# Performance work log

Measured on AMD Instinct MI355X. Metric: run time of the kernel, lower is better.

Reference implementation:

```python
import jax, jax.numpy as jnp
import numpy as np

N, E, IN_DIM, H, C, ED = 100000, 1600000, 128, 8, 16, 16
LN_EPS = 1e-5


def setup_inputs() -> dict:
    key = jax.random.key(0)
    ks = jax.random.split(key, 12)
    s_in = 1.0 / np.sqrt(IN_DIM)
    s_ed = 1.0 / np.sqrt(ED)
    return {
        "edge_index": jax.random.randint(ks[0], (2, E), 0, N, dtype=jnp.int64),
        "point_attr": jax.random.normal(ks[1], (N, IN_DIM), dtype=jnp.float32),
        "edge_attr": jax.random.normal(ks[2], (E, ED), dtype=jnp.float32),
        "W": jax.random.normal(ks[3], (IN_DIM, H * C), dtype=jnp.float32) * s_in,
        "att_src": jax.random.normal(ks[4], (1, H, C), dtype=jnp.float32) * 0.1,
        "att_dst": jax.random.normal(ks[5], (1, H, C), dtype=jnp.float32) * 0.1,
        "W_edge": jax.random.normal(ks[6], (ED, H * C), dtype=jnp.float32) * s_ed,
        "att_edge": jax.random.normal(ks[7], (1, H, C), dtype=jnp.float32) * 0.1,
        "bias": jnp.zeros((H * C,), dtype=jnp.float32),
        "ln_node_g": jnp.ones((H * C,), dtype=jnp.float32),
        "ln_node_b": jnp.zeros((H * C,), dtype=jnp.float32),
        "ln_edge_g": jnp.ones((H,), dtype=jnp.float32),
        "ln_edge_b": jnp.zeros((H,), dtype=jnp.float32),
        "edge_w": jax.random.normal(ks[8], (H, 1), dtype=jnp.float32) / np.sqrt(H),
        "edge_b": jnp.zeros((1,), dtype=jnp.float32),
    }


def _layer_norm(x, g, b):
    mu = jnp.mean(x, axis=-1, keepdims=True)
    var = jnp.mean((x - mu) ** 2, axis=-1, keepdims=True)
    return (x - mu) * jax.lax.rsqrt(var + LN_EPS) * g + b


def reference(edge_index, point_attr, edge_attr, W, att_src, att_dst, W_edge,
              att_edge, bias, ln_node_g, ln_node_b, ln_edge_g, ln_edge_b,
              edge_w, edge_b):
    src, dst = edge_index[0], edge_index[1]
    x = (point_attr @ W).reshape(N, H, C)                 # [N,H,C]
    a_src = jnp.sum(x * att_src, axis=-1)                 # [N,H]
    a_dst = jnp.sum(x * att_dst, axis=-1)                 # [N,H]
    e = (edge_attr @ W_edge).reshape(E, H, C)             # [E,H,C]
    a_edge = jnp.sum(e * att_edge, axis=-1)               # [E,H]
    alpha = jax.nn.leaky_relu(a_src[src] + a_dst[dst] + a_edge, 0.2)
    # segment softmax over destination neighborhoods
    m = jax.ops.segment_max(alpha, dst, num_segments=N)
    m = jnp.where(jnp.isfinite(m), m, 0.0)
    ex = jnp.exp(alpha - m[dst])
    den = jax.ops.segment_sum(ex, dst, num_segments=N)
    alpha_n = ex / (den[dst] + 1e-16)                     # [E,H]
    msg = x[src] * alpha_n[..., None]                     # [E,H,C]
    out = jax.ops.segment_sum(msg, dst, num_segments=N).reshape(N, H * C) + bias
    node_out = jax.nn.leaky_relu(_layer_norm(out, ln_node_g, ln_node_b), 0.01)
    edge_h = _layer_norm(alpha_n, ln_edge_g, ln_edge_b)
    edge_out = jax.nn.relu(edge_h @ edge_w + edge_b)[:, 0]  # [E]
    return node_out, edge_out
```

## Files before the change

kernel.cpp:

```cpp
#include <hip/hip_runtime.h>
#include <hip/hip_bf16.h>

#define NN 100000
#define EE 1600000
#define LN_EPS 1e-5f

__device__ __forceinline__ float bf_lo(unsigned u) {
  union { unsigned i; float f; } c; c.i = u << 16; return c.f;
}
__device__ __forceinline__ float bf_hi(unsigned u) {
  union { unsigned i; float f; } c; c.i = u & 0xffff0000u; return c.f;
}
__device__ __forceinline__ float us_bf(unsigned short u) {
  union { unsigned i; float f; } c; c.i = ((unsigned)u) << 16; return c.f;
}
__device__ __forceinline__ unsigned short f2bf(float f) {
  union { float f; unsigned i; } c; c.f = f;
  unsigned b = c.i + 0x7fffu + ((c.i >> 16) & 1u);
  return (unsigned short)(b >> 16);
}
__device__ __forceinline__ float lrelu02(float v) { return v >= 0.f ? v : 0.2f * v; }

__global__ void k_detect(const void* __restrict__ ei, int* __restrict__ flag) {
  if (threadIdx.x == 0 && blockIdx.x == 0) {
    const unsigned long long* p = (const unsigned long long*)ei;
    int ok = 1;
    for (int i = 0; i < 256; ++i)
      if (p[i] >= (unsigned long long)NN) { ok = 0; break; }
    *flag = ok;
  }
}

__global__ __launch_bounds__(256) void k_convert_hist(const void* __restrict__ ei,
                                                      const int* __restrict__ flag,
                                                      int* __restrict__ idx32,
                                                      int* __restrict__ counts) {
  int gid = blockIdx.x * 256 + threadIdx.x;
  if (gid >= EE) return;
  int i0 = gid * 2;
  int v0, v1;
  if (*flag) {
    longlong2 lv = *(const longlong2*)((const long long*)ei + i0);
    v0 = (int)lv.x; v1 = (int)lv.y;
  } else {
    int2 iv = *(const int2*)((const int*)ei + i0);
    v0 = iv.x; v1 = iv.y;
  }
  *(int2*)(idx32 + i0) = make_int2(v0, v1);
  if (i0 >= EE) {
    atomicAdd(&counts[v0], 1);
    atomicAdd(&counts[v1], 1);
  }
}

__global__ __launch_bounds__(512) void k_gemm_node(
    const float* __restrict__ P, const float* __restrict__ W,
    const float* __restrict__ attS, const float* __restrict__ attD,
    unsigned* __restrict__ xb, unsigned short* __restrict__ a_srcb,
    unsigned short* __restrict__ a_dstb, int nrows) {
  __shared__ float Rl[32 * 66];
  int t = threadIdx.x;
  int w = __builtin_amdgcn_readfirstlane(t >> 6);
  int l = t & 63;
  int rb = blockIdx.x * 64;
  int cb = w * 16;
  float acc[16];
#pragma unroll
  for (int j = 0; j < 16; ++j) acc[j] = 0.f;

  for (int kc = 0; kc < 4; ++kc) {
    __syncthreads();
    {
      int row = t >> 3;
      int k0 = (t & 7) * 4;
      int grow = rb + row;
      float4 v = make_float4(0.f, 0.f, 0.f, 0.f);
      if (grow < nrows)
        v = *(const float4*)(P + (size_t)grow * 128 + kc * 32 + k0);
      Rl[(k0 + 0) * 66 + row] = v.x;
      Rl[(k0 + 1) * 66 + row] = v.y;
      Rl[(k0 + 2) * 66 + row] = v.z;
      Rl[(k0 + 3) * 66 + row] = v.w;
    }
    __syncthreads();
    const float* Wp = W + (size_t)(kc * 32) * 128 + cb;
#pragma unroll 8
    for (int k = 0; k < 32; ++k) {
      float rv = Rl[k * 66 + l];
#pragma unroll
      for (int j = 0; j < 16; ++j) acc[j] = fmaf(rv, Wp[k * 128 + j], acc[j]);
    }
  }
  int row = rb + l;
  if (row < nrows) {
    float sa = 0.f, sd = 0.f;
#pragma unroll
    for (int j = 0; j < 16; ++j) {
      sa = fmaf(acc[j], attS[cb + j], sa);
      sd = fmaf(acc[j], attD[cb + j], sd);
    }
    a_srcb[(size_t)row * 8 + w] = f2bf(sa);
    a_dstb[(size_t)row * 8 + w] = f2bf(sd);
    unsigned pk[8];
#pragma unroll
    for (int m = 0; m < 8; ++m)
      pk[m] = (unsigned)f2bf(acc[2 * m]) | ((unsigned)f2bf(acc[2 * m + 1]) << 16);
    unsigned* xo = xb + (size_t)row * 64 + cb / 2;
    *(uint4*)(xo) = make_uint4(pk[0], pk[1], pk[2], pk[3]);
    *(uint4*)(xo + 4) = make_uint4(pk[4], pk[5], pk[6], pk[7]);
  }
}

__global__ __launch_bounds__(256) void k_blocksum(const int* __restrict__ counts,
                                                  int* __restrict__ partials, int n) {
  __shared__ int sm[256];
  int t = threadIdx.x;
  int gid = blockIdx.x * 256 + t;
  sm[t] = gid < n ? counts[gid] : 0;
  __syncthreads();
  for (int s = 128; s > 0; s >>= 1) {
    if (t < s) sm[t] += sm[t + s];
    __syncthreads();
  }
  if (t == 0) partials[blockIdx.x] = sm[0];
}

__global__ __launch_bounds__(512) void k_scanpartials(int* __restrict__ partials, int nb) {
  __shared__ int sm[512];
  int t = threadIdx.x;
  int v = t < nb ? partials[t] : 0;
  sm[t] = v;
  __syncthreads();
  for (int off = 1; off < 512; off <<= 1) {
    int u = (t >= off) ? sm[t - off] : 0;
    __syncthreads();
    sm[t] += u;
    __syncthreads();
  }
  if (t < nb) partials[t] = sm[t] - v;
}

__global__ __launch_bounds__(256) void k_scanfinal(const int* __restrict__ counts,
                                                   const int* __restrict__ partials,
                                                   int* __restrict__ offsets,
                                                   int* __restrict__ cursor, int n) {
  __shared__ int sm[256];
  int t = threadIdx.x;
  int gid = blockIdx.x * 256 + t;
  int v = gid < n ? counts[gid] : 0;
  sm[t] = v;
  __syncthreads();
  for (int off = 1; off < 256; off <<= 1) {
    int u = (t >= off) ? sm[t - off] : 0;
    __syncthreads();
    sm[t] += u;
    __syncthreads();
  }
  int excl = partials[blockIdx.x] + sm[t] - v;
  if (gid < n) {
    offsets[gid] = excl;
    cursor[gid] = excl;
  }
  if (gid == n - 1) offsets[n] = excl + v;
}

__global__ __launch_bounds__(256) void k_edgeprep(
    const float* __restrict__ EA, const float* __restrict__ Wedge,
    const float* __restrict__ attE, const int* __restrict__ src,
    const int* __restrict__ dst, const unsigned short* __restrict__ a_srcb,
    int* __restrict__ cursor, unsigned* __restrict__ rec,
    unsigned* __restrict__ asumb) {
  __shared__ float M[16][8];
  int t = threadIdx.x;
  if (t < 128) {
    int d = t >> 3, h = t & 7;
    float s = 0.f;
#pragma unroll
    for (int c = 0; c < 16; ++c)
      s = fmaf(Wedge[d * 128 + h * 16 + c], attE[h * 16 + c], s);
    M[d][h] = s;
  }
  __syncthreads();
  int e = blockIdx.x * 256 + t;
  if (e >= EE) return;
  float ea[16];
  const float4* ea4 = (const float4*)(EA + (size_t)e * 16);
#pragma unroll
  for (int i = 0; i < 4; ++i) {
    float4 v = ea4[i];
    ea[i * 4] = v.x; ea[i * 4 + 1] = v.y; ea[i * 4 + 2] = v.z; ea[i * 4 + 3] = v.w;
  }
  int sv = src[e], dv = dst[e];
  uint4 as4 = *(const uint4*)(a_srcb + (unsigned)sv * 8);
  unsigned asu[4] = {as4.x, as4.y, as4.z, as4.w};
  unsigned pk[4];
#pragma unroll
  for (int m = 0; m < 4; ++m) {
    float s0 = 0.f, s1 = 0.f;
#pragma unroll
    for (int d = 0; d < 16; ++d) {
      s0 = fmaf(ea[d], M[d][2 * m], s0);
      s1 = fmaf(ea[d], M[d][2 * m + 1], s1);
    }
    s0 += bf_lo(asu[m]);
    s1 += bf_hi(asu[m]);
    pk[m] = (unsigned)f2bf(s0) | ((unsigned)f2bf(s1) << 16);
  }
  uint4 asum = make_uint4(pk[0], pk[1], pk[2], pk[3]);
  *(uint4*)(asumb + (size_t)e * 4) = asum;
  int pos = atomicAdd(&cursor[dv], 1);
  unsigned* rp = rec + (size_t)pos * 8;
  *(uint4*)(rp) = asum;
  *(uint4*)(rp + 4) = make_uint4((unsigned)sv, (unsigned)e, 0u, 0u);
}

__global__ __launch_bounds__(512) void k_megaagg(
    const int* __restrict__ offsets, const unsigned* __restrict__ rec,
    const unsigned short* __restrict__ a_dstb, const unsigned* __restrict__ xb,
    const float* __restrict__ bias, const float* __restrict__ g,
    const float* __restrict__ b, float* __restrict__ node_out,
    float* __restrict__ inv_arr) {
  int w = threadIdx.x >> 6, l = threadIdx.x & 63;
  int n = blockIdx.x * 8 + w;
  if (n >= NN) return;
  int s = offsets[n], e = offsets[n + 1];
  int qt = l >> 4, ql = l & 15;
  int h = ql >> 1;
  int hsel = (ql >> 1) & 1;
  int hw = ql >> 2;
  float ad = us_bf(a_dstb[(unsigned)n * 8 + h]);
  float dn0 = 0.f, dn1 = 0.f;
  float acc[8] = {0.f, 0.f, 0.f, 0.f, 0.f, 0.f, 0.f, 0.f};
  int i = s + qt;
  for (; i + 4 < e; i += 8) {
    unsigned auA = rec[(size_t)i * 8 + hw];
    int svA = (int)rec[(size_t)i * 8 + 4];
    unsigned auB = rec[(size_t)(i + 4) * 8 + hw];
    int svB = (int)rec[(size_t)(i + 4) * 8 + 4];
    uint4 xA = *(const uint4*)(xb + (unsigned)svA * 64 + ql * 4);
    uint4 xB = *(const uint4*)(xb + (unsigned)svB * 64 + ql * 4);
    float aA = hsel ? bf_hi(auA) : bf_lo(auA);
    float aB = hsel ? bf_hi(auB) : bf_lo(auB);
    float eA = __expf(lrelu02(aA + ad));
    float eB = __expf(lrelu02(aB + ad));
    dn0 += eA; dn1 += eB;
    acc[0] = fmaf(eA, bf_lo(xA.x), acc[0]);
    acc[1] = fmaf(eA, bf_hi(xA.x), acc[1]);
    acc[2] = fmaf(eA, bf_lo(xA.y), acc[2]);
    acc[3] = fmaf(eA, bf_hi(xA.y), acc[3]);
    acc[4] = fmaf(eA, bf_lo(xA.z), acc[4]);
    acc[5] = fmaf(eA, bf_hi(xA.z), acc[5]);
    acc[6] = fmaf(eA, bf_lo(xA.w), acc[6]);
    acc[7] = fmaf(eA, bf_hi(xA.w), acc[7]);
    acc[0] = fmaf(eB, bf_lo(xB.x), acc[0]);
    acc[1] = fmaf(eB, bf_hi(xB.x), acc[1]);
    acc[2] = fmaf(eB, bf_lo(xB.y), acc[2]);
    acc[3] = fmaf(eB, bf_hi(xB.y), acc[3]);
    acc[4] = fmaf(eB, bf_lo(xB.z), acc[4]);
    acc[5] = fmaf(eB, bf_hi(xB.z), acc[5]);
    acc[6] = fmaf(eB, bf_lo(xB.w), acc[6]);
    acc[7] = fmaf(eB, bf_hi(xB.w), acc[7]);
  }
  if (i < e) {
    unsigned auA = rec[(size_t)i * 8 + hw];
    int svA = (int)rec[(size_t)i * 8 + 4];
    uint4 xA = *(const uint4*)(xb + (unsigned)svA * 64 + ql * 4);
    float aA = hsel ? bf_hi(auA) : bf_lo(auA);
    float eA = __expf(lrelu02(aA + ad));
    dn0 += eA;
    acc[0] = fmaf(eA, bf_lo(xA.x), acc[0]);
    acc[1] = fmaf(eA, bf_hi(xA.x), acc[1]);
    acc[2] = fmaf(eA, bf_lo(xA.y), acc[2]);
    acc[3] = fmaf(eA, bf_hi(xA.y), acc[3]);
    acc[4] = fmaf(eA, bf_lo(xA.z), acc[4]);
    acc[5] = fmaf(eA, bf_hi(xA.z), acc[5]);
    acc[6] = fmaf(eA, bf_lo(xA.w), acc[6]);
    acc[7] = fmaf(eA, bf_hi(xA.w), acc[7]);
  }
  float den = dn0 + dn1;
  den += __shfl_xor(den, 16);
  den += __shfl_xor(den, 32);
#pragma unroll
  for (int j = 0; j < 8; ++j) {
    acc[j] += __shfl_xor(acc[j], 16);
    acc[j] += __shfl_xor(acc[j], 32);
  }
  float inv = 1.f / (den + 1e-16f);
  if (qt == 0 && (ql & 1) == 0) inv_arr[(unsigned)n * 8 + h] = inv;
  int c0 = ql * 8;
  float4 bv0 = *(const float4*)(bias + c0);
  float4 bv1 = *(const float4*)(bias + c0 + 4);
  acc[0] = acc[0] * inv + bv0.x;
  acc[1] = acc[1] * inv + bv0.y;
  acc[2] = acc[2] * inv + bv0.z;
  acc[3] = acc[3] * inv + bv0.w;
  acc[4] = acc[4] * inv + bv1.x;
  acc[5] = acc[5] * inv + bv1.y;
  acc[6] = acc[6] * inv + bv1.z;
  acc[7] = acc[7] * inv + bv1.w;
  float sum = ((acc[0] + acc[1]) + (acc[2] + acc[3])) +
              ((acc[4] + acc[5]) + (acc[6] + acc[7]));
#pragma unroll
  for (int off = 1; off < 64; off <<= 1) sum += __shfl_xor(sum, off);
  float mu = sum * (1.f / 512.f);
  float d[8], ss = 0.f;
#pragma unroll
  for (int j = 0; j < 8; ++j) { d[j] = acc[j] - mu; ss += d[j] * d[j]; }
#pragma unroll
  for (int off = 1; off < 64; off <<= 1) ss += __shfl_xor(ss, off);
  float r = rsqrtf(ss * (1.f / 512.f) + LN_EPS);
  if (qt == 0) {
    float4 gv0 = *(const float4*)(g + c0);
    float4 gv1 = *(const float4*)(g + c0 + 4);
    float4 bb0 = *(const float4*)(b + c0);
    float4 bb1 = *(const float4*)(b + c0 + 4);
    float y[8];
    y[0] = d[0] * r * gv0.x + bb0.x;
    y[1] = d[1] * r * gv0.y + bb0.y;
    y[2] = d[2] * r * gv0.z + bb0.z;
    y[3] = d[3] * r * gv0.w + bb0.w;
    y[4] = d[4] * r * gv1.x + bb1.x;
    y[5] = d[5] * r * gv1.y + bb1.y;
    y[6] = d[6] * r * gv1.z + bb1.z;
    y[7] = d[7] * r * gv1.w + bb1.w;
#pragma unroll
    for (int j = 0; j < 8; ++j) y[j] = y[j] >= 0.f ? y[j] : 0.01f * y[j];
    float* no = node_out + (size_t)n * 128 + c0;
    *(float4*)(no) = make_float4(y[0], y[1], y[2], y[3]);
    *(float4*)(no + 4) = make_float4(y[4], y[5], y[6], y[7]);
  }
}

__global__ __launch_bounds__(256) void k_edgeout(
    const unsigned* __restrict__ asumb, const unsigned short* __restrict__ a_dstb,
    const int* __restrict__ dst, const float* __restrict__ inv_arr,
    const float* __restrict__ g, const float* __restrict__ b,
    const float* __restrict__ ew, const float* __restrict__ eb,
    float* __restrict__ edge_out) {
  int gid = blockIdx.x * 256 + threadIdx.x;
  if (gid * 2 >= EE) return;
  int i0 = gid * 2;
  float gl[8], bl[8], wl[8];
#pragma unroll
  for (int h = 0; h < 8; ++h) { gl[h] = g[h]; bl[h] = b[h]; wl[h] = ew[h]; }
  float ebv = eb[0];
  int2 dvs = *(const int2*)(dst + i0);
  float out2[2];
#pragma unroll
  for (int u = 0; u < 2; ++u) {
    int i = i0 + u;
    int dv = (u == 0) ? dvs.x : dvs.y;
    uint4 as4 = *(const uint4*)(asumb + (size_t)i * 4);
    uint4 ad4 = *(const uint4*)(a_dstb + (unsigned)dv * 8);
    const float4* iv4 = (const float4*)(inv_arr + (unsigned)dv * 8);
    float4 iv0 = iv4[0], iv1 = iv4[1];
    float iv[8] = {iv0.x, iv0.y, iv0.z, iv0.w, iv1.x, iv1.y, iv1.z, iv1.w};
    unsigned asu[4] = {as4.x, as4.y, as4.z, as4.w};
    unsigned adu[4] = {ad4.x, ad4.y, ad4.z, ad4.w};
    float p[8];
#pragma unroll
    for (int m = 0; m < 4; ++m) {
      float a0 = lrelu02(bf_lo(asu[m]) + bf_lo(adu[m]));
      float a1 = lrelu02(bf_hi(asu[m]) + bf_hi(adu[m]));
      p[2 * m] = __expf(a0) * iv[2 * m];
      p[2 * m + 1] = __expf(a1) * iv[2 * m + 1];
    }
    float mu = 0.f;
#pragma unroll
    for (int h = 0; h < 8; ++h) mu += p[h];
    mu *= 0.125f;
    float var = 0.f;
#pragma unroll
    for (int h = 0; h < 8; ++h) { float dd = p[h] - mu; var += dd * dd; }
    var *= 0.125f;
    float r = rsqrtf(var + LN_EPS);
    float o = ebv;
#pragma unroll
    for (int h = 0; h < 8; ++h)
      o += ((p[h] - mu) * r * gl[h] + bl[h]) * wl[h];
    out2[u] = fmaxf(o, 0.f);
  }
  *(float2*)(edge_out + i0) = make_float2(out2[0], out2[1]);
}

extern "C" void kernel_launch(void* const* d_in, const int* in_sizes, int n_in,
                              void* d_out, int out_size, void* d_ws, size_t ws_size,
                              hipStream_t stream) {
  const void* edge_index = d_in[0];
  const float* point_attr = (const float*)d_in[1];
  const float* edge_attr = (const float*)d_in[2];
  const float* W = (const float*)d_in[3];
  const float* att_src = (const float*)d_in[4];
  const float* att_dst = (const float*)d_in[5];
  const float* W_edge = (const float*)d_in[6];
  const float* att_edge = (const float*)d_in[7];
  const float* bias = (const float*)d_in[8];
  const float* ln_node_g = (const float*)d_in[9];
  const float* ln_node_b = (const float*)d_in[10];
  const float* ln_edge_g = (const float*)d_in[11];
  const float* ln_edge_b = (const float*)d_in[12];
  const float* edge_w = (const float*)d_in[13];
  const float* edge_b = (const float*)d_in[14];

  char* wsb = (char*)d_ws;
  size_t o = 0;
  auto take = [&](size_t bytes) -> void* {
    void* p = wsb + o;
    o += (bytes + 255) & ~(size_t)255;
    return p;
  };
  int* flag = (int*)take(4);
  int* idx32 = (int*)take((size_t)2 * EE * 4);
  unsigned* xb = (unsigned*)take((size_t)NN * 128 * 2);
  unsigned short* a_srcb = (unsigned short*)take((size_t)NN * 8 * 2);
  unsigned short* a_dstb = (unsigned short*)take((size_t)NN * 8 * 2);
  int* counts = (int*)take((size_t)NN * 4);
  int* offsets = (int*)take((size_t)(NN + 1) * 4);
  int* cursor = (int*)take((size_t)NN * 4);
  int* partials = (int*)take(512 * 4);
  unsigned* rec = (unsigned*)take((size_t)EE * 32);
  unsigned* asumb = (unsigned*)take((size_t)EE * 16);
  float* inv_arr = (float*)take((size_t)NN * 8 * 4);

  const int* srcp = idx32;
  const int* dstp = idx32 + EE;
  float* node_out = (float*)d_out;
  float* edge_out = node_out + (size_t)NN * 128;

  int nb_scan = (NN + 255) / 256;

  hipMemsetAsync(counts, 0, (size_t)NN * 4, stream);

  k_detect<<<1, 64, 0, stream>>>(edge_index, flag);
  k_convert_hist<<<(EE + 255) / 256, 256, 0, stream>>>(edge_index, flag, idx32, counts);
  k_gemm_node<<<(NN + 63) / 64, 512, 0, stream>>>(point_attr, W, att_src, att_dst,
                                                  xb, a_srcb, a_dstb, NN);
  k_blocksum<<<nb_scan, 256, 0, stream>>>(counts, partials, NN);
  k_scanpartials<<<1, 512, 0, stream>>>(partials, nb_scan);
  k_scanfinal<<<nb_scan, 256, 0, stream>>>(counts, partials, offsets, cursor, NN);
  k_edgeprep<<<(EE + 255) / 256, 256, 0, stream>>>(edge_attr, W_edge, att_edge, srcp,
                                                   dstp, a_srcb, cursor, rec, asumb);
  k_megaagg<<<(NN + 7) / 8, 512, 0, stream>>>(offsets, rec, a_dstb, xb, bias,
                                              ln_node_g, ln_node_b, node_out, inv_arr);
  k_edgeout<<<(EE / 2 + 255) / 256, 256, 0, stream>>>(asumb, a_dstb, dstp, inv_arr,
                                                      ln_edge_g, ln_edge_b, edge_w,
                                                      edge_b, edge_out);
}
```

Baseline: 355.8 us.

## Drop asumb buffer, read CSR records in edgeout, process two edges per thread

Edge prep now handles two edges per thread, issues the cursor atomics early, and writes only the CSR-ordered record, which now also stores the destination index. The separate per-edge asumb array is removed. The edge-output kernel reads records sequentially in CSR order and scatters its result to edge_out[e], which gives coherent reads of the gathered inputs by dst but uncoalesced 4-byte output writes. The aggregation loop is unrolled to four edges per lane group to get more gathers in flight.

```diff
diff --git a/kernel.cpp b/kernel.cpp
--- a/kernel.cpp
+++ b/kernel.cpp
@@ -168,8 +168,7 @@
     const float* __restrict__ EA, const float* __restrict__ Wedge,
     const float* __restrict__ attE, const int* __restrict__ src,
     const int* __restrict__ dst, const unsigned short* __restrict__ a_srcb,
-    int* __restrict__ cursor, unsigned* __restrict__ rec,
-    unsigned* __restrict__ asumb) {
+    int* __restrict__ cursor, unsigned* __restrict__ rec) {
   __shared__ float M[16][8];
   int t = threadIdx.x;
   if (t < 128) {
@@ -181,37 +180,51 @@
     M[d][h] = s;
   }
   __syncthreads();
-  int e = blockIdx.x * 256 + t;
-  if (e >= EE) return;
-  float ea[16];
-  const float4* ea4 = (const float4*)(EA + (size_t)e * 16);
+  int gid = blockIdx.x * 256 + t;
+  int i0 = gid * 2;
+  if (i0 >= EE) return;
+  int2 svs = *(const int2*)(src + i0);
+  int2 dvs = *(const int2*)(dst + i0);
+  int pos0 = atomicAdd(&cursor[dvs.x], 1);
+  int pos1 = atomicAdd(&cursor[dvs.y], 1);
+  uint4 as0 = *(const uint4*)(a_srcb + (unsigned)svs.x * 8);
+  uint4 as1 = *(const uint4*)(a_srcb + (unsigned)svs.y * 8);
+  float ea0[16], ea1[16];
+  const float4* e4 = (const float4*)(EA + (size_t)i0 * 16);
 #pragma unroll
   for (int i = 0; i < 4; ++i) {
-    float4 v = ea4[i];
-    ea[i * 4] = v.x; ea[i * 4 + 1] = v.y; ea[i * 4 + 2] = v.z; ea[i * 4 + 3] = v.w;
-  }
-  int sv = src[e], dv = dst[e];
-  uint4 as4 = *(const uint4*)(a_srcb + (unsigned)sv * 8);
-  unsigned asu[4] = {as4.x, as4.y, as4.z, as4.w};
-  unsigned pk[4];
+    float4 v = e4[i];
+    ea0[i * 4] = v.x; ea0[i * 4 + 1] = v.y; ea0[i * 4 + 2] = v.z; ea0[i * 4 + 3] = v.w;
+  }
+#pragma unroll
+  for (int i = 0; i < 4; ++i) {
+    float4 v = e4[4 + i];
+    ea1[i * 4] = v.x; ea1[i * 4 + 1] = v.y; ea1[i * 4 + 2] = v.z; ea1[i * 4 + 3] = v.w;
+  }
+  unsigned asu0[4] = {as0.x, as0.y, as0.z, as0.w};
+  unsigned asu1[4] = {as1.x, as1.y, as1.z, as1.w};
+  unsigned pk0[4], pk1[4];
 #pragma unroll
   for (int m = 0; m < 4; ++m) {
-    float s0 = 0.f, s1 = 0.f;
+    float a0 = 0.f, a1 = 0.f, b0 = 0.f, b1 = 0.f;
 #pragma unroll
     for (int d = 0; d < 16; ++d) {
-      s0 = fmaf(ea[d], M[d][2 * m], s0);
-      s1 = fmaf(ea[d], M[d][2 * m + 1], s1);
+      a0 = fmaf(ea0[d], M[d][2 * m], a0);
+      a1 = fmaf(ea0[d], M[d][2 * m + 1], a1);
+      b0 = fmaf(ea1[d], M[d][2 * m], b0);
+      b1 = fmaf(ea1[d], M[d][2 * m + 1], b1);
     }
-    s0 += bf_lo(asu[m]);
-    s1 += bf_hi(asu[m]);
-    pk[m] = (unsigned)f2bf(s0) | ((unsigned)f2bf(s1) << 16);
-  }
-  uint4 asum = make_uint4(pk[0], pk[1], pk[2], pk[3]);
-  *(uint4*)(asumb + (size_t)e * 4) = asum;
-  int pos = atomicAdd(&cursor[dv], 1);
-  unsigned* rp = rec + (size_t)pos * 8;
-  *(uint4*)(rp) = asum;
-  *(uint4*)(rp + 4) = make_uint4((unsigned)sv, (unsigned)e, 0u, 0u);
+    a0 += bf_lo(asu0[m]); a1 += bf_hi(asu0[m]);
+    b0 += bf_lo(asu1[m]); b1 += bf_hi(asu1[m]);
+    pk0[m] = (unsigned)f2bf(a0) | ((unsigned)f2bf(a1) << 16);
+    pk1[m] = (unsigned)f2bf(b0) | ((unsigned)f2bf(b1) << 16);
+  }
+  unsigned* rp0 = rec + (size_t)pos0 * 8;
+  *(uint4*)(rp0) = make_uint4(pk0[0], pk0[1], pk0[2], pk0[3]);
+  *(uint4*)(rp0 + 4) = make_uint4((unsigned)svs.x, (unsigned)i0, (unsigned)dvs.x, 0u);
+  unsigned* rp1 = rec + (size_t)pos1 * 8;
+  *(uint4*)(rp1) = make_uint4(pk1[0], pk1[1], pk1[2], pk1[3]);
+  *(uint4*)(rp1 + 4) = make_uint4((unsigned)svs.y, (unsigned)(i0 + 1), (unsigned)dvs.y, 0u);
 }
 
 __global__ __launch_bounds__(512) void k_megaagg(
@@ -229,55 +242,61 @@
   int hsel = (ql >> 1) & 1;
   int hw = ql >> 2;
   float ad = us_bf(a_dstb[(unsigned)n * 8 + h]);
-  float dn0 = 0.f, dn1 = 0.f;
+  float dn0 = 0.f, dn1 = 0.f, dn2 = 0.f, dn3 = 0.f;
   float acc[8] = {0.f, 0.f, 0.f, 0.f, 0.f, 0.f, 0.f, 0.f};
   int i = s + qt;
-  for (; i + 4 < e; i += 8) {
-    unsigned auA = rec[(size_t)i * 8 + hw];
-    int svA = (int)rec[(size_t)i * 8 + 4];
-    unsigned auB = rec[(size_t)(i + 4) * 8 + hw];
-    int svB = (int)rec[(size_t)(i + 4) * 8 + 4];
+  for (; i + 12 < e; i += 16) {
+    const unsigned* rA = rec + (size_t)i * 8;
+    const unsigned* rB = rec + (size_t)(i + 4) * 8;
+    const unsigned* rC = rec + (size_t)(i + 8) * 8;
+    const unsigned* rD = rec + (size_t)(i + 12) * 8;
+    unsigned auA = rA[hw]; int svA = (int)rA[4];
+    unsigned auB = rB[hw]; int svB = (int)rB[4];
+    unsigned auC = rC[hw]; int svC = (int)rC[4];
+    unsigned auD = rD[hw]; int svD = (int)rD[4];
     uint4 xA = *(const uint4*)(xb + (unsigned)svA * 64 + ql * 4);
     uint4 xB = *(const uint4*)(xb + (unsigned)svB * 64 + ql * 4);
+    uint4 xC = *(const uint4*)(xb + (unsigned)svC * 64 + ql * 4);
+    uint4 xD = *(const uint4*)(xb + (unsigned)svD * 64 + ql * 4);
     float aA = hsel ? bf_hi(auA) : bf_lo(auA);
     float aB = hsel ? bf_hi(auB) : bf_lo(auB);
+    float aC = hsel ? bf_hi(auC) : bf_lo(auC);
+    float aD = hsel ? bf_hi(auD) : bf_lo(auD);
     float eA = __expf(lrelu02(aA + ad));
     float eB = __expf(lrelu02(aB + ad));
-    dn0 += eA; dn1 += eB;
-    acc[0] = fmaf(eA, bf_lo(xA.x), acc[0]);
-    acc[1] = fmaf(eA, bf_hi(xA.x), acc[1]);
-    acc[2] = fmaf(eA, bf_lo(xA.y), acc[2]);
-    acc[3] = fmaf(eA, bf_hi(xA.y), acc[3]);
-    acc[4] = fmaf(eA, bf_lo(xA.z), acc[4]);
-    acc[5] = fmaf(eA, bf_hi(xA.z), acc[5]);
-    acc[6] = fmaf(eA, bf_lo(xA.w), acc[6]);
-    acc[7] = fmaf(eA, bf_hi(xA.w), acc[7]);
-    acc[0] = fmaf(eB, bf_lo(xB.x), acc[0]);
-    acc[1] = fmaf(eB, bf_hi(xB.x), acc[1]);
-    acc[2] = fmaf(eB, bf_lo(xB.y), acc[2]);
-    acc[3] = fmaf(eB, bf_hi(xB.y), acc[3]);
-    acc[4] = fmaf(eB, bf_lo(xB.z), acc[4]);
-    acc[5] = fmaf(eB, bf_hi(xB.z), acc[5]);
-    acc[6] = fmaf(eB, bf_lo(xB.w), acc[6]);
-    acc[7] = fmaf(eB, bf_hi(xB.w), acc[7]);
-  }
-  if (i < e) {
-    unsigned auA = rec[(size_t)i * 8 + hw];
-    int svA = (int)rec[(size_t)i * 8 + 4];
+    float eC = __expf(lrelu02(aC + ad));
+    float eD = __expf(lrelu02(aD + ad));
+    dn0 += eA; dn1 += eB; dn2 += eC; dn3 += eD;
+    acc[0] = fmaf(eA, bf_lo(xA.x), acc[0]); acc[1] = fmaf(eA, bf_hi(xA.x), acc[1]);
+    acc[2] = fmaf(eA, bf_lo(xA.y), acc[2]); acc[3] = fmaf(eA, bf_hi(xA.y), acc[3]);
+    acc[4] = fmaf(eA, bf_lo(xA.z), acc[4]); acc[5] = fmaf(eA, bf_hi(xA.z), acc[5]);
+    acc[6] = fmaf(eA, bf_lo(xA.w), acc[6]); acc[7] = fmaf(eA, bf_hi(xA.w), acc[7]);
+    acc[0] = fmaf(eB, bf_lo(xB.x), acc[0]); acc[1] = fmaf(eB, bf_hi(xB.x), acc[1]);
+    acc[2] = fmaf(eB, bf_lo(xB.y), acc[2]); acc[3] = fmaf(eB, bf_hi(xB.y), acc[3]);
+    acc[4] = fmaf(eB, bf_lo(xB.z), acc[4]); acc[5] = fmaf(eB, bf_hi(xB.z), acc[5]);
+    acc[6] = fmaf(eB, bf_lo(xB.w), acc[6]); acc[7] = fmaf(eB, bf_hi(xB.w), acc[7]);
+    acc[0] = fmaf(eC, bf_lo(xC.x), acc[0]); acc[1] = fmaf(eC, bf_hi(xC.x), acc[1]);
+    acc[2] = fmaf(eC, bf_lo(xC.y), acc[2]); acc[3] = fmaf(eC, bf_hi(xC.y), acc[3]);
+    acc[4] = fmaf(eC, bf_lo(xC.z), acc[4]); acc[5] = fmaf(eC, bf_hi(xC.z), acc[5]);
+    acc[6] = fmaf(eC, bf_lo(xC.w), acc[6]); acc[7] = fmaf(eC, bf_hi(xC.w), acc[7]);
+    acc[0] = fmaf(eD, bf_lo(xD.x), acc[0]); acc[1] = fmaf(eD, bf_hi(xD.x), acc[1]);
+    acc[2] = fmaf(eD, bf_lo(xD.y), acc[2]); acc[3] = fmaf(eD, bf_hi(xD.y), acc[3]);
+    acc[4] = fmaf(eD, bf_lo(xD.z), acc[4]); acc[5] = fmaf(eD, bf_hi(xD.z), acc[5]);
+    acc[6] = fmaf(eD, bf_lo(xD.w), acc[6]); acc[7] = fmaf(eD, bf_hi(xD.w), acc[7]);
+  }
+  for (; i < e; i += 4) {
+    const unsigned* rA = rec + (size_t)i * 8;
+    unsigned auA = rA[hw]; int svA = (int)rA[4];
     uint4 xA = *(const uint4*)(xb + (unsigned)svA * 64 + ql * 4);
     float aA = hsel ? bf_hi(auA) : bf_lo(auA);
     float eA = __expf(lrelu02(aA + ad));
     dn0 += eA;
-    acc[0] = fmaf(eA, bf_lo(xA.x), acc[0]);
-    acc[1] = fmaf(eA, bf_hi(xA.x), acc[1]);
-    acc[2] = fmaf(eA, bf_lo(xA.y), acc[2]);
-    acc[3] = fmaf(eA, bf_hi(xA.y), acc[3]);
-    acc[4] = fmaf(eA, bf_lo(xA.z), acc[4]);
-    acc[5] = fmaf(eA, bf_hi(xA.z), acc[5]);
-    acc[6] = fmaf(eA, bf_lo(xA.w), acc[6]);
-    acc[7] = fmaf(eA, bf_hi(xA.w), acc[7]);
-  }
-  float den = dn0 + dn1;
+    acc[0] = fmaf(eA, bf_lo(xA.x), acc[0]); acc[1] = fmaf(eA, bf_hi(xA.x), acc[1]);
+    acc[2] = fmaf(eA, bf_lo(xA.y), acc[2]); acc[3] = fmaf(eA, bf_hi(xA.y), acc[3]);
+    acc[4] = fmaf(eA, bf_lo(xA.z), acc[4]); acc[5] = fmaf(eA, bf_hi(xA.z), acc[5]);
+    acc[6] = fmaf(eA, bf_lo(xA.w), acc[6]); acc[7] = fmaf(eA, bf_hi(xA.w), acc[7]);
+  }
+  float den = (dn0 + dn1) + (dn2 + dn3);
   den += __shfl_xor(den, 16);
   den += __shfl_xor(den, 32);
 #pragma unroll
@@ -332,25 +351,23 @@
 }
 
 __global__ __launch_bounds__(256) void k_edgeout(
-    const unsigned* __restrict__ asumb, const unsigned short* __restrict__ a_dstb,
-    const int* __restrict__ dst, const float* __restrict__ inv_arr,
-    const float* __restrict__ g, const float* __restrict__ b,
-    const float* __restrict__ ew, const float* __restrict__ eb,
-    float* __restrict__ edge_out) {
+    const unsigned* __restrict__ rec, const unsigned short* __restrict__ a_dstb,
+    const float* __restrict__ inv_arr, const float* __restrict__ g,
+    const float* __restrict__ b, const float* __restrict__ ew,
+    const float* __restrict__ eb, float* __restrict__ edge_out) {
   int gid = blockIdx.x * 256 + threadIdx.x;
   if (gid * 2 >= EE) return;
-  int i0 = gid * 2;
   float gl[8], bl[8], wl[8];
 #pragma unroll
   for (int h = 0; h < 8; ++h) { gl[h] = g[h]; bl[h] = b[h]; wl[h] = ew[h]; }
   float ebv = eb[0];
-  int2 dvs = *(const int2*)(dst + i0);
-  float out2[2];
 #pragma unroll
   for (int u = 0; u < 2; ++u) {
-    int i = i0 + u;
-    int dv = (u == 0) ? dvs.x : dvs.y;
-    uint4 as4 = *(const uint4*)(asumb + (size_t)i * 4);
+    const unsigned* rp = rec + (size_t)(gid * 2 + u) * 8;
+    uint4 as4 = *(const uint4*)(rp);
+    uint4 hi4 = *(const uint4*)(rp + 4);
+    int e = (int)hi4.y;
+    int dv = (int)hi4.z;
     uint4 ad4 = *(const uint4*)(a_dstb + (unsigned)dv * 8);
     const float4* iv4 = (const float4*)(inv_arr + (unsigned)dv * 8);
     float4 iv0 = iv4[0], iv1 = iv4[1];
@@ -378,9 +395,8 @@
 #pragma unroll
     for (int h = 0; h < 8; ++h)
       o += ((p[h] - mu) * r * gl[h] + bl[h]) * wl[h];
-    out2[u] = fmaxf(o, 0.f);
-  }
-  *(float2*)(edge_out + i0) = make_float2(out2[0], out2[1]);
+    edge_out[e] = fmaxf(o, 0.f);
+  }
 }
 
 extern "C" void kernel_launch(void* const* d_in, const int* in_sizes, int n_in,
@@ -419,7 +435,6 @@
   int* cursor = (int*)take((size_t)NN * 4);
   int* partials = (int*)take(512 * 4);
   unsigned* rec = (unsigned*)take((size_t)EE * 32);
-  unsigned* asumb = (unsigned*)take((size_t)EE * 16);
   float* inv_arr = (float*)take((size_t)NN * 8 * 4);
 
   const int* srcp = idx32;
@@ -438,11 +453,11 @@
   k_blocksum<<<nb_scan, 256, 0, stream>>>(counts, partials, NN);
   k_scanpartials<<<1, 512, 0, stream>>>(partials, nb_scan);
   k_scanfinal<<<nb_scan, 256, 0, stream>>>(counts, partials, offsets, cursor, NN);
-  k_edgeprep<<<(EE + 255) / 256, 256, 0, stream>>>(edge_attr, W_edge, att_edge, srcp,
-                                                   dstp, a_srcb, cursor, rec, asumb);
+  k_edgeprep<<<(EE / 2 + 255) / 256, 256, 0, stream>>>(edge_attr, W_edge, att_edge,
+                                                       srcp, dstp, a_srcb, cursor, rec);
   k_megaagg<<<(NN + 7) / 8, 512, 0, stream>>>(offsets, rec, a_dstb, xb, bias,
                                               ln_node_g, ln_node_b, node_out, inv_arr);
-  k_edgeout<<<(EE / 2 + 255) / 256, 256, 0, stream>>>(asumb, a_dstb, dstp, inv_arr,
+  k_edgeout<<<(EE / 2 + 255) / 256, 256, 0, stream>>>(rec, a_dstb, inv_arr,
                                                       ln_edge_g, ln_edge_b, edge_w,
                                                       edge_b, edge_out);
 }
```

New measurement: 373.1 us. +4.9%, slower.
